# Performance work log

Hardware: AMD Instinct MI355X
Metric: run time of the kernel (lower is better)

The kernel has to match this reference:

```python
import jax, jax.numpy as jnp
import numpy as np

N = 100000; E = 1600000; D_IN = 128; HID = 64; HEADS = 2; OUT = 2; B = 8192
NEG_SLOPE = 0.2


def gat_conv(x, edge_index, W, a_src, a_dst, bias):
    """PyG-style GATConv with add_self_loops=True, concat=False (mean over heads).
    x: [N, Fin], W: [Fin, H*C], a_src/a_dst: [H, C], bias: [C]."""
    n = x.shape[0]
    H, C = a_src.shape
    h = (x @ W).reshape(n, H, C)                      # [N,H,C]
    s_src = (h * a_src[None]).sum(-1)                 # [N,H]
    s_dst = (h * a_dst[None]).sum(-1)                 # [N,H]
    loop = jnp.arange(n, dtype=edge_index.dtype)
    src = jnp.concatenate([edge_index[0], loop])      # [E+N]
    dst = jnp.concatenate([edge_index[1], loop])
    e = jax.nn.leaky_relu(s_src[src] + s_dst[dst], NEG_SLOPE)   # [E+N,H]
    # segment softmax over edges grouped by destination node
    m = jax.ops.segment_max(e, dst, num_segments=n)             # [N,H]
    ex = jnp.exp(e - m[dst])
    z = jax.ops.segment_sum(ex, dst, num_segments=n)            # [N,H]
    alpha = ex / z[dst]                                          # [E+N,H]
    msg = h[src] * alpha[:, :, None]                             # [E+N,H,C]
    out = jax.ops.segment_sum(msg, dst, num_segments=n)         # [N,H,C]
    return out.mean(axis=1) + bias                               # concat=False -> mean over heads


def setup_inputs() -> dict:
    key = jax.random.key(0)
    ks = jax.random.split(key, 32)
    def p(k, shape, fan_in):
        return (jax.random.normal(k, shape, dtype=jnp.float32) / np.sqrt(fan_in)).astype(jnp.float32)
    inp = {}
    inp["x_l"] = jax.random.normal(ks[0], (N, D_IN), dtype=jnp.float32)
    inp["x_r"] = jax.random.normal(ks[1], (N, D_IN), dtype=jnp.float32)
    inp["edge_index_l"] = jax.random.randint(ks[2], (2, E), 0, N, dtype=jnp.int64 if jax.config.jax_enable_x64 else jnp.int32)
    inp["edge_index_r"] = jax.random.randint(ks[3], (2, E), 0, N, dtype=jnp.int64 if jax.config.jax_enable_x64 else jnp.int32)
    inp["labels_l"] = jax.random.randint(ks[4], (B,), 0, N)
    inp["labels_r"] = jax.random.randint(ks[5], (B,), 0, N)
    i = 6
    for side in ("l", "r"):
        inp[f"w1{side}"] = p(ks[i], (D_IN, HEADS * HID), D_IN); i += 1
        inp[f"as1{side}"] = p(ks[i], (HEADS, HID), HID); i += 1
        inp[f"ad1{side}"] = p(ks[i], (HEADS, HID), HID); i += 1
        inp[f"b1{side}"] = jnp.zeros((HID,), jnp.float32)
        inp[f"w2{side}"] = p(ks[i], (HID, HEADS * HID), HID); i += 1
        inp[f"as2{side}"] = p(ks[i], (HEADS, HID), HID); i += 1
        inp[f"ad2{side}"] = p(ks[i], (HEADS, HID), HID); i += 1
        inp[f"b2{side}"] = jnp.zeros((HID,), jnp.float32)
    inp["fc1_w"] = p(ks[i], (2 * HID, HID), 2 * HID); i += 1
    inp["fc1_b"] = jnp.zeros((HID,), jnp.float32)
    inp["fc2_w"] = p(ks[i], (HID, OUT), HID); i += 1
    inp["fc2_b"] = jnp.zeros((OUT,), jnp.float32)
    return inp


def reference(x_l, x_r, edge_index_l, edge_index_r, labels_l, labels_r,
              w1l, as1l, ad1l, b1l, w2l, as2l, ad2l, b2l,
              w1r, as1r, ad1r, b1r, w2r, as2r, ad2r, b2r,
              fc1_w, fc1_b, fc2_w, fc2_b):
    # left tower (dropout is identity in eval mode)
    hl = jax.nn.relu(gat_conv(x_l, edge_index_l, w1l, as1l, ad1l, b1l))
    hl = jax.nn.relu(gat_conv(hl, edge_index_l, w2l, as2l, ad2l, b2l))
    # right tower
    hr = jax.nn.relu(gat_conv(x_r, edge_index_r, w1r, as1r, ad1r, b1r))
    hr = jax.nn.relu(gat_conv(hr, edge_index_r, w2r, as2r, ad2r, b2r))
    # merge_graphs: gather node features per labeled pair, concat
    merged = jnp.concatenate([hl[labels_l], hr[labels_r]], axis=-1)  # [B, 2*HID]
    x = jax.nn.relu(merged @ fc1_w + fc1_b)
    return x @ fc2_w + fc2_b
```

## Files before the change

### kernel.cpp

```cpp
#include <hip/hip_runtime.h>
#include <hip/hip_bf16.h>
#include <hip/hip_fp16.h>

constexpr int NN   = 100000;
constexpr int EE   = 1600000;
constexpr int BB   = 8192;
constexpr int PAD  = 48;
constexpr float NEG_SLOPE = 0.2f;

constexpr int GBM = 128;
constexpr int GB = (NN + GBM - 1) / GBM;
constexpr int AB2 = NN / 8;

constexpr int BSPAN = 256;
constexpr int NB    = (NN + BSPAN - 1) / BSPAN;
constexpr int BCAP  = 5120;
constexpr int CHA   = 2048;
constexpr int NCH   = (EE + CHA - 1) / CHA;

typedef _Float16 f16x8 __attribute__((ext_vector_type(8)));
typedef _Float16 f16x4 __attribute__((ext_vector_type(4)));
typedef float    f32x4 __attribute__((ext_vector_type(4)));

__device__ __forceinline__ float4 ld4(const float* p) { return *(const float4*)p; }

template <typename TIN, int K>
__device__ __forceinline__
void gemm_mfma_body(int bid, const TIN* __restrict__ x,
                    const __half* __restrict__ Wimg,
                    const float* __restrict__ a_src, const float* __restrict__ a_dst,
                    __half* __restrict__ h,
                    float* __restrict__ ssrc, float* __restrict__ sdst,
                    char* lds) {
    constexpr bool HAS_LO = sizeof(TIN) == 4;
    char* const xh = lds;
    char* const xl = HAS_LO ? (lds + 8192) : lds;
    char* const wh = lds + (HAS_LO ? 16384 : 8192);
    char* const wl = wh + 8192;

    const int tid = threadIdx.x;
    const int wid = tid >> 6;
    const int lane = tid & 63;
    const int l15 = lane & 15;
    const int lg = lane >> 4;
    const int row0 = bid * GBM;

    f32x4 acc[2][8];
    #pragma unroll
    for (int i = 0; i < 2; ++i)
        #pragma unroll
        for (int j = 0; j < 8; ++j) acc[i][j] = (f32x4)0.f;

    for (int kt = 0; kt < K; kt += 32) {
        __syncthreads();
        if constexpr (HAS_LO) {
            #pragma unroll
            for (int i = 0; i < 4; ++i) {
                int idx = tid + i * 256;
                int row = idx >> 3, c4 = idx & 7;
                int grow = row0 + row; if (grow >= NN) grow = NN - 1;
                float4 v = ld4(&x[(size_t)grow * K + kt + c4 * 4]);
                f16x4 hv, lv;
                float f0 = v.x; _Float16 h0 = (_Float16)f0; hv[0] = h0; lv[0] = (_Float16)(f0 - (float)h0);
                float f1 = v.y; _Float16 h1 = (_Float16)f1; hv[1] = h1; lv[1] = (_Float16)(f1 - (float)h1);
                float f2 = v.z; _Float16 h2 = (_Float16)f2; hv[2] = h2; lv[2] = (_Float16)(f2 - (float)h2);
                float f3 = v.w; _Float16 h3 = (_Float16)f3; hv[3] = h3; lv[3] = (_Float16)(f3 - (float)h3);
                int byt = row * 64 + ((c4 * 8) ^ ((row & 3) << 4));
                *(f16x4*)(xh + byt) = hv;
                *(f16x4*)(xl + byt) = lv;
            }
        } else {
            #pragma unroll
            for (int i = 0; i < 2; ++i) {
                int idx = tid + i * 256;
                int row = idx >> 2, c8 = idx & 3;
                int grow = row0 + row; if (grow >= NN) grow = NN - 1;
                uint4 v = *(const uint4*)&x[(size_t)grow * 64 + kt + c8 * 8];
                int byt = row * 64 + ((c8 * 16) ^ ((row & 3) << 4));
                *(uint4*)(xh + byt) = v;
            }
        }
        {
            const uint4* ws = (const uint4*)((const char*)Wimg + (size_t)(kt >> 5) * 16384);
            uint4* wd = (uint4*)wh;
            #pragma unroll
            for (int i = 0; i < 4; ++i) wd[tid + i * 256] = ws[tid + i * 256];
        }
        __syncthreads();

        const int koff = lg * 16;
        f16x8 ah[2], al[2];
        #pragma unroll
        for (int rt = 0; rt < 2; ++rt) {
            int row = wid * 32 + rt * 16 + l15;
            int byt = row * 64 + (koff ^ ((row & 3) << 4));
            ah[rt] = *(const f16x8*)(xh + byt);
            if constexpr (HAS_LO) al[rt] = *(const f16x8*)(xl + byt);
        }
        #pragma unroll
        for (int ct = 0; ct < 8; ++ct) {
            int col = ct * 16 + l15;
            int byt = col * 64 + (koff ^ ((col & 3) << 4));
            f16x8 bh = *(const f16x8*)(wh + byt);
            f16x8 bl = *(const f16x8*)(wl + byt);
            #pragma unroll
            for (int rt = 0; rt < 2; ++rt) {
                acc[rt][ct] = __builtin_amdgcn_mfma_f32_16x16x32_f16(ah[rt], bh, acc[rt][ct], 0, 0, 0);
                acc[rt][ct] = __builtin_amdgcn_mfma_f32_16x16x32_f16(ah[rt], bl, acc[rt][ct], 0, 0, 0);
                if constexpr (HAS_LO)
                    acc[rt][ct] = __builtin_amdgcn_mfma_f32_16x16x32_f16(al[rt], bh, acc[rt][ct], 0, 0, 0);
            }
        }
    }

    float sv[8], dv[8];
    #pragma unroll
    for (int ct = 0; ct < 8; ++ct) {
        sv[ct] = a_src[ct * 16 + l15];
        dv[ct] = a_dst[ct * 16 + l15];
    }
    #pragma unroll
    for (int rt = 0; rt < 2; ++rt) {
        #pragma unroll
        for (int r = 0; r < 4; ++r) {
            int row = row0 + wid * 32 + rt * 16 + lg * 4 + r;
            bool ok = row < NN;
            if (ok) {
                #pragma unroll
                for (int ct = 0; ct < 8; ++ct)
                    h[(size_t)row * 128 + ct * 16 + l15] = __float2half(acc[rt][ct][r]);
            }
            float ps0 = 0.f, pd0 = 0.f, ps1 = 0.f, pd1 = 0.f;
            #pragma unroll
            for (int ct = 0; ct < 4; ++ct) {
                ps0 = fmaf(acc[rt][ct][r], sv[ct], ps0);
                pd0 = fmaf(acc[rt][ct][r], dv[ct], pd0);
                ps1 = fmaf(acc[rt][ct + 4][r], sv[ct + 4], ps1);
                pd1 = fmaf(acc[rt][ct + 4][r], dv[ct + 4], pd1);
            }
            ps0 += __shfl_xor(ps0, 1); pd0 += __shfl_xor(pd0, 1);
            ps1 += __shfl_xor(ps1, 1); pd1 += __shfl_xor(pd1, 1);
            ps0 += __shfl_xor(ps0, 2); pd0 += __shfl_xor(pd0, 2);
            ps1 += __shfl_xor(ps1, 2); pd1 += __shfl_xor(pd1, 2);
            ps0 += __shfl_xor(ps0, 4); pd0 += __shfl_xor(pd0, 4);
            ps1 += __shfl_xor(ps1, 4); pd1 += __shfl_xor(pd1, 4);
            ps0 += __shfl_xor(ps0, 8); pd0 += __shfl_xor(pd0, 8);
            ps1 += __shfl_xor(ps1, 8); pd1 += __shfl_xor(pd1, 8);
            if (ok && l15 == 0) {
                ssrc[row * 2 + 0] = ps0;
                ssrc[row * 2 + 1] = ps1;
                sdst[row * 2 + 0] = pd0;
                sdst[row * 2 + 1] = pd1;
            }
        }
    }
}

__global__ __launch_bounds__(256)
void k_bucket(const int* __restrict__ el, const int* __restrict__ er,
              int* __restrict__ buf, int* __restrict__ gcur,
              const float* __restrict__ w1l, const float* __restrict__ w1r,
              const float* __restrict__ w2l, const float* __restrict__ w2r,
              __half* __restrict__ wi1l, __half* __restrict__ wi1r,
              __half* __restrict__ wi2l, __half* __restrict__ wi2r) {
    const int blk0 = blockIdx.x;
    if (blk0 >= 2 * NCH) {
        const int id = blk0 - 2 * NCH;
        const float* W;
        __half* img;
        int kt;
        if (id < 8) {
            W = (id >> 2) ? w1r : w1l;
            img = ((id >> 2) ? wi1r : wi1l) + (size_t)(id & 3) * 8192;
            kt = (id & 3) * 32;
        } else {
            int jx = id - 8;
            W = (jx >> 1) ? w2r : w2l;
            img = ((jx >> 1) ? wi2r : wi2l) + (size_t)(jx & 1) * 8192;
            kt = (jx & 1) * 32;
        }
        _Float16* imgh = (_Float16*)img;
        _Float16* imgl = imgh + 4096;
        for (int i = threadIdx.x; i < 4096; i += 256) {
            int kk = i >> 7, col = i & 127;
            float f = W[(size_t)(kt + kk) * 128 + col];
            _Float16 hi = (_Float16)f;
            _Float16 lo = (_Float16)(f - (float)hi);
            int hidx = col * 32 + (kk ^ ((col & 3) << 3));
            imgh[hidx] = hi;
            imgl[hidx] = lo;
        }
        return;
    }

    __shared__ int   P1[CHA];
    __shared__ short bkof[CHA];
    __shared__ int hist[NB];
    __shared__ int st[NB];
    __shared__ int ofs[NB];
    __shared__ int base[NB];
    __shared__ int sc[512];

    const int blk = blk0;
    const bool right = blk >= NCH;
    const int* __restrict__ e = right ? er : el;
    const int sideoff = right ? NB : 0;
    const int cbase = (right ? blk - NCH : blk) * CHA;
    int cnum = EE - cbase; if (cnum > CHA) cnum = CHA;
    const int t = threadIdx.x;

    for (int i = t; i < NB; i += 256) hist[i] = 0;
    __syncthreads();
    for (int i = t; i < cnum; i += 256) {
        int d = e[EE + cbase + i];
        atomicAdd(&hist[d >> 8], 1);
    }
    __syncthreads();

    sc[t]       = (t < NB)       ? hist[t]       : 0;
    sc[t + 256] = (t + 256 < NB) ? hist[t + 256] : 0;
    __syncthreads();
    for (int off = 1; off < 512; off <<= 1) {
        int a0 = sc[t];
        int a1 = sc[t + 256];
        int b0 = (t >= off)       ? sc[t - off]       : 0;
        int b1 = (t + 256 >= off) ? sc[t + 256 - off] : 0;
        __syncthreads();
        sc[t] = a0 + b0;
        sc[t + 256] = a1 + b1;
        __syncthreads();
    }
    for (int i = t; i < NB; i += 256) {
        int s = sc[i] - hist[i];
        st[i] = s;
        ofs[i] = s;
    }
    __syncthreads();
    for (int i = t; i < cnum; i += 256) {
        int d = e[EE + cbase + i];
        int s = e[cbase + i];
        int bk = d >> 8;
        int pos = atomicAdd(&ofs[bk], 1);
        P1[pos] = (s << 8) | (d & 255);
        bkof[pos] = (short)bk;
    }
    __syncthreads();
    for (int i = t; i < NB; i += 256)
        base[i] = hist[i] ? atomicAdd(&gcur[sideoff + i], hist[i]) : 0;
    __syncthreads();
    for (int j = t; j < cnum; j += 256) {
        int bk = bkof[j];
        buf[(size_t)(sideoff + bk) * BCAP + base[bk] + (j - st[bk])] = P1[j];
    }
}

__device__ __forceinline__
void csr_body(int blk, const int* __restrict__ buf, const int* __restrict__ gcur,
              int* __restrict__ cntl, int* __restrict__ cntr,
              int* __restrict__ csrl, int* __restrict__ csrr, char* smem) {
    int* lcnt = (int*)smem;
    int* lcsr = (int*)(smem + 1024);

    const bool right = blk >= NB;
    const int bk = right ? blk - NB : blk;
    int* __restrict__ cnt = right ? cntr : cntl;
    int* __restrict__ csr = right ? csrr : csrl;
    const int* __restrict__ src = buf + (size_t)blk * BCAP;
    const int count = gcur[blk];
    const int lo = bk * BSPAN;
    int nn = NN - lo; if (nn > BSPAN) nn = BSPAN;
    const int t = threadIdx.x;

    for (int i = t; i < nn; i += 256) lcnt[i] = 0;
    __syncthreads();
    for (int i = t; i < count; i += 256) {
        int v = src[i];
        int ld = v & 255;
        int s  = (int)((unsigned)v >> 8);
        int slot = atomicAdd(&lcnt[ld], 1);
        lcsr[ld * PAD + slot] = s;
    }
    __syncthreads();
    const int tot4 = (nn * PAD) >> 2;
    int4* __restrict__ dst4 = (int4*)&csr[(size_t)lo * PAD];
    const int4* __restrict__ s4 = (const int4*)lcsr;
    for (int i = t; i < tot4; i += 256) dst4[i] = s4[i];
    for (int i = t; i < nn; i += 256) cnt[lo + i] = lcnt[i];
}

__global__ __launch_bounds__(256)
void k_csr_gemm1(const int* __restrict__ buf, const int* __restrict__ gcur,
                 int* __restrict__ cnt_l, int* __restrict__ cnt_r,
                 int* __restrict__ csr_l, int* __restrict__ csr_r,
                 const float* __restrict__ x_l, const float* __restrict__ x_r,
                 const __half* __restrict__ wi1l, const float* __restrict__ as1l,
                 const float* __restrict__ ad1l,
                 const __half* __restrict__ wi1r, const float* __restrict__ as1r,
                 const float* __restrict__ ad1r,
                 __half* __restrict__ h_l, __half* __restrict__ h_r,
                 float* __restrict__ ssrc_l, float* __restrict__ sdst_l,
                 float* __restrict__ ssrc_r, float* __restrict__ sdst_r) {
    __shared__ __align__(16) char smem[50176];
    int b = blockIdx.x;
    if (b < 2 * NB) {
        csr_body(b, buf, gcur, cnt_l, cnt_r, csr_l, csr_r, smem);
    } else {
        b -= 2 * NB;
        if (b < GB)
            gemm_mfma_body<float, 128>(b, x_l, wi1l, as1l, ad1l,
                                       h_l, ssrc_l, sdst_l, smem);
        else
            gemm_mfma_body<float, 128>(b - GB, x_r, wi1r, as1r, ad1r,
                                       h_r, ssrc_r, sdst_r, smem);
    }
}

__global__ __launch_bounds__(256)
void k_gemm2x(const __half* __restrict__ f_l, const __half* __restrict__ f_r,
              const __half* __restrict__ wi2l, const float* __restrict__ as2l,
              const float* __restrict__ ad2l,
              const __half* __restrict__ wi2r, const float* __restrict__ as2r,
              const float* __restrict__ ad2r,
              __half* __restrict__ h_l, __half* __restrict__ h_r,
              float* __restrict__ ssrc_l, float* __restrict__ sdst_l,
              float* __restrict__ ssrc_r, float* __restrict__ sdst_r) {
    __shared__ __align__(16) char smem[24576];
    int b = blockIdx.x;
    if (b < GB)
        gemm_mfma_body<__half, 64>(b, (const __half*)f_l, wi2l, as2l, ad2l,
                                   h_l, ssrc_l, sdst_l, smem);
    else
        gemm_mfma_body<__half, 64>(b - GB, (const __half*)f_r, wi2r, as2r, ad2r,
                                   h_r, ssrc_r, sdst_r, smem);
}

__device__ __forceinline__
void att_body(int n, const __half* __restrict__ h,
              const float* __restrict__ ssrc, const float* __restrict__ sdst,
              const int* __restrict__ cnt, const int* __restrict__ csr,
              const float* __restrict__ bias, __half* __restrict__ out) {
    const int g  = threadIdx.x & 31;
    const int hs = g >> 4;
    const int j  = g & 15;
    const int ch = g * 4;

    float sd = sdst[n * 2 + hs];
    float es = ssrc[n * 2 + hs] + sd;
    es = es > 0.f ? es : NEG_SLOPE * es;
    const float wself = __expf(es);
    float zl = 0.f;

    uint2 sv = *(const uint2*)&h[(size_t)n * 128 + ch];
    __half2 sh0 = *(__half2*)&sv.x, sh1 = *(__half2*)&sv.y;
    float2 p01 = __half22float2(sh0), p23 = __half22float2(sh1);
    float a0 = wself * p01.x, a1 = wself * p01.y;
    float a2 = wself * p23.x, a3 = wself * p23.y;

    int b = n * PAD;
    const int e = b + cnt[n];
    while (b < e) {
        int c = e - b; if (c > 16) c = 16;
        int idx = b + (j < c ? j : c - 1);
        int sj = csr[idx];
        float ev = ssrc[sj * 2 + hs] + sd;
        ev = ev > 0.f ? ev : NEG_SLOPE * ev;
        float w = (j < c) ? __expf(ev) : 0.f;
        zl += w;
        int jj = 0;
        for (; jj + 4 <= c; jj += 4) {
            int s0 = __shfl(sj, jj,     32);
            int s1 = __shfl(sj, jj + 1, 32);
            int s2 = __shfl(sj, jj + 2, 32);
            int s3 = __shfl(sj, jj + 3, 32);
            float w0 = __shfl(w, hs * 16 + jj,     32);
            float w1 = __shfl(w, hs * 16 + jj + 1, 32);
            float w2 = __shfl(w, hs * 16 + jj + 2, 32);
            float w3 = __shfl(w, hs * 16 + jj + 3, 32);
            uint2 u0 = *(const uint2*)&h[(size_t)(unsigned)(s0 * 128 + ch)];
            uint2 u1 = *(const uint2*)&h[(size_t)(unsigned)(s1 * 128 + ch)];
            uint2 u2 = *(const uint2*)&h[(size_t)(unsigned)(s2 * 128 + ch)];
            uint2 u3 = *(const uint2*)&h[(size_t)(unsigned)(s3 * 128 + ch)];
            float2 f0a = __half22float2(*(__half2*)&u0.x), f0b = __half22float2(*(__half2*)&u0.y);
            float2 f1a = __half22float2(*(__half2*)&u1.x), f1b = __half22float2(*(__half2*)&u1.y);
            float2 f2a = __half22float2(*(__half2*)&u2.x), f2b = __half22float2(*(__half2*)&u2.y);
            float2 f3a = __half22float2(*(__half2*)&u3.x), f3b = __half22float2(*(__half2*)&u3.y);
            a0 = fmaf(w0, f0a.x, a0); a1 = fmaf(w0, f0a.y, a1);
            a2 = fmaf(w0, f0b.x, a2); a3 = fmaf(w0, f0b.y, a3);
            a0 = fmaf(w1, f1a.x, a0); a1 = fmaf(w1, f1a.y, a1);
            a2 = fmaf(w1, f1b.x, a2); a3 = fmaf(w1, f1b.y, a3);
            a0 = fmaf(w2, f2a.x, a0); a1 = fmaf(w2, f2a.y, a1);
            a2 = fmaf(w2, f2b.x, a2); a3 = fmaf(w2, f2b.y, a3);
            a0 = fmaf(w3, f3a.x, a0); a1 = fmaf(w3, f3a.y, a1);
            a2 = fmaf(w3, f3b.x, a2); a3 = fmaf(w3, f3b.y, a3);
        }
        for (; jj < c; ++jj) {
            int s0   = __shfl(sj, jj, 32);
            float w0 = __shfl(w, hs * 16 + jj, 32);
            uint2 u0 = *(const uint2*)&h[(size_t)(unsigned)(s0 * 128 + ch)];
            float2 f0a = __half22float2(*(__half2*)&u0.x), f0b = __half22float2(*(__half2*)&u0.y);
            a0 = fmaf(w0, f0a.x, a0); a1 = fmaf(w0, f0a.y, a1);
            a2 = fmaf(w0, f0b.x, a2); a3 = fmaf(w0, f0b.y, a3);
        }
        b += c;
    }

    zl += __shfl_xor(zl, 1, 32);
    zl += __shfl_xor(zl, 2, 32);
    zl += __shfl_xor(zl, 4, 32);
    zl += __shfl_xor(zl, 8, 32);
    const float z = wself + zl;

    float zi = 1.f / z;
    a0 *= zi; a1 *= zi; a2 *= zi; a3 *= zi;
    a0 = 0.5f * (a0 + __shfl_xor(a0, 16));
    a1 = 0.5f * (a1 + __shfl_xor(a1, 16));
    a2 = 0.5f * (a2 + __shfl_xor(a2, 16));
    a3 = 0.5f * (a3 + __shfl_xor(a3, 16));
    if (hs == 0) {
        float4 bv = *(const float4*)&bias[ch];
        a0 += bv.x; a1 += bv.y; a2 += bv.z; a3 += bv.w;
        a0 = a0 > 0.f ? a0 : 0.f;
        a1 = a1 > 0.f ? a1 : 0.f;
        a2 = a2 > 0.f ? a2 : 0.f;
        a3 = a3 > 0.f ? a3 : 0.f;
        __align__(8) __half2 hp[2];
        hp[0] = __floats2half2_rn(a0, a1);
        hp[1] = __floats2half2_rn(a2, a3);
        *(uint2*)&out[(size_t)n * 64 + ch] = *(uint2*)hp;
    }
}

__global__ __launch_bounds__(256)
void k_att2x(const __half* __restrict__ h_l, const __half* __restrict__ h_r,
             const float* __restrict__ ssrc_l, const float* __restrict__ sdst_l,
             const float* __restrict__ ssrc_r, const float* __restrict__ sdst_r,
             const int* __restrict__ cnt_l, const int* __restrict__ csr_l,
             const int* __restrict__ cnt_r, const int* __restrict__ csr_r,
             const float* __restrict__ bias_l, const float* __restrict__ bias_r,
             __half* __restrict__ feat_l, __half* __restrict__ feat_r) {
    int blk = blockIdx.x;
    bool right = blk >= AB2;
    int n = (blk - (right ? AB2 : 0)) * 8 + (threadIdx.x >> 5);
    if (!right) att_body(n, h_l, ssrc_l, sdst_l, cnt_l, csr_l, bias_l, feat_l);
    else        att_body(n, h_r, ssrc_r, sdst_r, cnt_r, csr_r, bias_r, feat_r);
}

__global__ __launch_bounds__(256)
void k_fc(const __half* __restrict__ fl, const __half* __restrict__ fr,
          const int* __restrict__ ll, const int* __restrict__ lr,
          const float* __restrict__ w1, const float* __restrict__ b1,
          const float* __restrict__ w2, const float* __restrict__ b2,
          float* __restrict__ out) {
    int b = blockIdx.x * 4 + (threadIdx.x >> 6);
    int j = threadIdx.x & 63;
    int la = ll[b], lb = lr[b];
    float v0 = __half2float(fl[(size_t)la * 64 + j]);
    float v1 = __half2float(fr[(size_t)lb * 64 + j]);
    float acc = b1[j];
    #pragma unroll 8
    for (int k = 0; k < 64; ++k)
        acc += __shfl(v0, k, 64) * w1[k * 64 + j];
    #pragma unroll 8
    for (int k = 0; k < 64; ++k)
        acc += __shfl(v1, k, 64) * w1[(64 + k) * 64 + j];
    float x1 = acc > 0.f ? acc : 0.f;
    float p0 = x1 * w2[j * 2 + 0];
    float p1 = x1 * w2[j * 2 + 1];
    #pragma unroll
    for (int o = 32; o >= 1; o >>= 1) {
        p0 += __shfl_xor(p0, o, 64);
        p1 += __shfl_xor(p1, o, 64);
    }
    if (j == 0) {
        out[b * 2 + 0] = p0 + b2[0];
        out[b * 2 + 1] = p1 + b2[1];
    }
}

extern "C" void kernel_launch(void* const* d_in, const int* in_sizes, int n_in,
                              void* d_out, int out_size, void* d_ws, size_t ws_size,
                              hipStream_t stream) {
    const float* x_l  = (const float*)d_in[0];
    const float* x_r  = (const float*)d_in[1];
    const int* ei_l  = (const int*)d_in[2];
    const int* ei_r  = (const int*)d_in[3];
    const int* lab_l = (const int*)d_in[4];
    const int* lab_r = (const int*)d_in[5];
    const float* w1l  = (const float*)d_in[6];
    const float* as1l = (const float*)d_in[7];
    const float* ad1l = (const float*)d_in[8];
    const float* b1l  = (const float*)d_in[9];
    const float* w2l  = (const float*)d_in[10];
    const float* as2l = (const float*)d_in[11];
    const float* ad2l = (const float*)d_in[12];
    const float* b2l  = (const float*)d_in[13];
    const float* w1r  = (const float*)d_in[14];
    const float* as1r = (const float*)d_in[15];
    const float* ad1r = (const float*)d_in[16];
    const float* b1r  = (const float*)d_in[17];
    const float* w2r  = (const float*)d_in[18];
    const float* as2r = (const float*)d_in[19];
    const float* ad2r = (const float*)d_in[20];
    const float* b2r  = (const float*)d_in[21];
    const float* fc1w = (const float*)d_in[22];
    const float* fc1b = (const float*)d_in[23];
    const float* fc2w = (const float*)d_in[24];
    const float* fc2b = (const float*)d_in[25];

    char* p = (char*)d_ws;
    auto alloc = [&](size_t bytes) -> void* {
        void* q = (void*)p;
        p += (bytes + 255) & ~(size_t)255;
        return q;
    };
    __half* h_l    = (__half*)alloc((size_t)NN * 128 * 2);
    __half* h_r    = (__half*)alloc((size_t)NN * 128 * 2);
    __half* feat_l = (__half*)alloc((size_t)NN * 64 * 2);
    __half* feat_r = (__half*)alloc((size_t)NN * 64 * 2);
    float* ssrc_l = (float*)alloc((size_t)NN * 2 * 4);
    float* sdst_l = (float*)alloc((size_t)NN * 2 * 4);
    float* ssrc_r = (float*)alloc((size_t)NN * 2 * 4);
    float* sdst_r = (float*)alloc((size_t)NN * 2 * 4);
    int* cnt2  = (int*)alloc(((size_t)2 * NN + 2 * NB) * 4);
    int* csr_l = (int*)alloc((size_t)NN * PAD * 4);
    int* csr_r = (int*)alloc((size_t)NN * PAD * 4);
    __half* wi1l = (__half*)alloc(65536);
    __half* wi1r = (__half*)alloc(65536);
    __half* wi2l = (__half*)alloc(32768);
    __half* wi2r = (__half*)alloc(32768);
    int* cnt_l = cnt2;
    int* cnt_r = cnt2 + NN;
    int* gcur  = cnt2 + 2 * NN;

    int* buf = (int*)feat_l;

    hipMemsetAsync(gcur, 0, (size_t)2 * NB * 4, stream);

    k_bucket<<<2 * NCH + 12, 256, 0, stream>>>(ei_l, ei_r, buf, gcur,
                                               w1l, w1r, w2l, w2r,
                                               wi1l, wi1r, wi2l, wi2r);

    k_csr_gemm1<<<2 * NB + 2 * GB, 256, 0, stream>>>(
        buf, gcur, cnt_l, cnt_r, csr_l, csr_r,
        x_l, x_r, wi1l, as1l, ad1l, wi1r, as1r, ad1r,
        h_l, h_r, ssrc_l, sdst_l, ssrc_r, sdst_r);

    k_att2x<<<2 * AB2, 256, 0, stream>>>(h_l, h_r, ssrc_l, sdst_l, ssrc_r, sdst_r,
                                         cnt_l, csr_l, cnt_r, csr_r,
                                         b1l, b1r, feat_l, feat_r);

    k_gemm2x<<<2 * GB, 256, 0, stream>>>(feat_l, feat_r,
                                         wi2l, as2l, ad2l, wi2r, as2r, ad2r,
                                         h_l, h_r, ssrc_l, sdst_l, ssrc_r, sdst_r);

    k_att2x<<<2 * AB2, 256, 0, stream>>>(h_l, h_r, ssrc_l, sdst_l, ssrc_r, sdst_r,
                                         cnt_l, csr_l, cnt_r, csr_r,
                                         b2l, b2r, feat_l, feat_r);

    k_fc<<<(BB + 3) / 4, 256, 0, stream>>>(feat_l, feat_r, lab_l, lab_r,
                                           fc1w, fc1b, fc2w, fc2b,
                                           (float*)d_out);
}
```

Measured before the change: 546.8 us.

## Fuse layer-1 attention aggregation with layer-2 GEMM via LDS staging

Adds a kernel that computes layer-1 GAT attention aggregation for a 64-row tile, writes the result as fp16 into swizzled shared memory, and immediately runs the layer-2 MFMA GEMM plus attention-score reduction on it. This removes the global round trip of the intermediate features and one kernel launch. The cost is a smaller GEMM tile, with the weight image reloaded for each 64-row block. The workspace needs extra buffers, so the old path is kept as a fallback when the workspace is too small.

```diff
diff --git a/kernel.cpp b/kernel.cpp
--- a/kernel.cpp
+++ b/kernel.cpp
@@ -10,6 +10,8 @@
 
 constexpr int GBM = 128;
 constexpr int GB = (NN + GBM - 1) / GBM;
+constexpr int GBM2 = 64;
+constexpr int GB2 = (NN + GBM2 - 1) / GBM2;
 constexpr int AB2 = NN / 8;
 
 constexpr int BSPAN = 256;
@@ -334,11 +336,13 @@
                                    h_r, ssrc_r, sdst_r, smem);
 }
 
+template <int WRITER>
 __device__ __forceinline__
-void att_body(int n, const __half* __restrict__ h,
-              const float* __restrict__ ssrc, const float* __restrict__ sdst,
-              const int* __restrict__ cnt, const int* __restrict__ csr,
-              const float* __restrict__ bias, __half* __restrict__ out) {
+void att_body_t(int n, int row_local, const __half* __restrict__ h,
+                const float* __restrict__ ssrc, const float* __restrict__ sdst,
+                const int* __restrict__ cnt, const int* __restrict__ csr,
+                const float* __restrict__ bias, __half* __restrict__ out,
+                char* featlds) {
     const int g  = threadIdx.x & 31;
     const int hs = g >> 4;
     const int j  = g & 15;
@@ -426,7 +430,14 @@
         __align__(8) __half2 hp[2];
         hp[0] = __floats2half2_rn(a0, a1);
         hp[1] = __floats2half2_rn(a2, a3);
-        *(uint2*)&out[(size_t)n * 64 + ch] = *(uint2*)hp;
+        if constexpr (WRITER == 0) {
+            *(uint2*)&out[(size_t)n * 64 + ch] = *(uint2*)hp;
+        } else {
+            int ph = ch >> 5;
+            int cc = ch & 31;
+            int byt = ph * (GBM2 * 64) + row_local * 64 + ((cc * 2) ^ ((row_local & 3) << 4));
+            *(uint2*)(featlds + byt) = *(uint2*)hp;
+        }
     }
 }
 
@@ -441,8 +452,137 @@
     int blk = blockIdx.x;
     bool right = blk >= AB2;
     int n = (blk - (right ? AB2 : 0)) * 8 + (threadIdx.x >> 5);
-    if (!right) att_body(n, h_l, ssrc_l, sdst_l, cnt_l, csr_l, bias_l, feat_l);
-    else        att_body(n, h_r, ssrc_r, sdst_r, cnt_r, csr_r, bias_r, feat_r);
+    if (!right) att_body_t<0>(n, 0, h_l, ssrc_l, sdst_l, cnt_l, csr_l, bias_l, feat_l, nullptr);
+    else        att_body_t<0>(n, 0, h_r, ssrc_r, sdst_r, cnt_r, csr_r, bias_r, feat_r, nullptr);
+}
+
+__global__ __launch_bounds__(256)
+void k_att1gemm2(const __half* __restrict__ h1_l, const __half* __restrict__ h1_r,
+                 const float* __restrict__ ss1_l, const float* __restrict__ sd1_l,
+                 const float* __restrict__ ss1_r, const float* __restrict__ sd1_r,
+                 const int* __restrict__ cnt_l, const int* __restrict__ csr_l,
+                 const int* __restrict__ cnt_r, const int* __restrict__ csr_r,
+                 const float* __restrict__ b1l, const float* __restrict__ b1r,
+                 const __half* __restrict__ wi2l, const float* __restrict__ as2l,
+                 const float* __restrict__ ad2l,
+                 const __half* __restrict__ wi2r, const float* __restrict__ as2r,
+                 const float* __restrict__ ad2r,
+                 __half* __restrict__ h2_l, __half* __restrict__ h2_r,
+                 float* __restrict__ ss2_l, float* __restrict__ sd2_l,
+                 float* __restrict__ ss2_r, float* __restrict__ sd2_r) {
+    __shared__ __align__(16) char smem[GBM2 * 64 * 2 + 16384];
+    char* const featp = smem;
+    char* const wh = smem + GBM2 * 64 * 2;
+    char* const wl = wh + 8192;
+
+    int b = blockIdx.x;
+    const bool right = b >= GB2;
+    const int bid = right ? b - GB2 : b;
+    const int row0 = bid * GBM2;
+
+    const __half* __restrict__ h1   = right ? h1_r : h1_l;
+    const float* __restrict__ ss1   = right ? ss1_r : ss1_l;
+    const float* __restrict__ sd1   = right ? sd1_r : sd1_l;
+    const int* __restrict__ cnt     = right ? cnt_r : cnt_l;
+    const int* __restrict__ csr     = right ? csr_r : csr_l;
+    const float* __restrict__ bias1 = right ? b1r : b1l;
+    const __half* __restrict__ Wimg = right ? wi2r : wi2l;
+    const float* __restrict__ a_src = right ? as2r : as2l;
+    const float* __restrict__ a_dst = right ? ad2r : ad2l;
+    __half* __restrict__ h2         = right ? h2_r : h2_l;
+    float* __restrict__ ss2         = right ? ss2_r : ss2_l;
+    float* __restrict__ sd2         = right ? sd2_r : sd2_l;
+
+    const int tid = threadIdx.x;
+
+    if (row0 + GBM2 > NN) {
+        for (int i = tid; i < (GBM2 * 64 * 2) / 16; i += 256)
+            ((uint4*)featp)[i] = make_uint4(0, 0, 0, 0);
+        __syncthreads();
+    }
+
+    #pragma unroll 1
+    for (int it = 0; it < GBM2 / 8; ++it) {
+        int nl = it * 8 + (tid >> 5);
+        int n = row0 + nl;
+        if (n < NN)
+            att_body_t<1>(n, nl, h1, ss1, sd1, cnt, csr, bias1, nullptr, featp);
+    }
+    __syncthreads();
+
+    const int wid = tid >> 6;
+    const int lane = tid & 63;
+    const int l15 = lane & 15;
+    const int lg = lane >> 4;
+
+    f32x4 acc[8];
+    #pragma unroll
+    for (int j = 0; j < 8; ++j) acc[j] = (f32x4)0.f;
+
+    #pragma unroll
+    for (int kp = 0; kp < 2; ++kp) {
+        if (kp) __syncthreads();
+        {
+            const uint4* ws = (const uint4*)((const char*)Wimg + (size_t)kp * 16384);
+            uint4* wd = (uint4*)wh;
+            #pragma unroll
+            for (int i = 0; i < 4; ++i) wd[tid + i * 256] = ws[tid + i * 256];
+        }
+        __syncthreads();
+
+        const int koff = lg * 16;
+        int row = wid * 16 + l15;
+        f16x8 ah = *(const f16x8*)(featp + kp * (GBM2 * 64) + row * 64 +
+                                   (koff ^ ((row & 3) << 4)));
+        #pragma unroll
+        for (int ct = 0; ct < 8; ++ct) {
+            int col = ct * 16 + l15;
+            int byt = col * 64 + (koff ^ ((col & 3) << 4));
+            f16x8 bh = *(const f16x8*)(wh + byt);
+            f16x8 bl = *(const f16x8*)(wl + byt);
+            acc[ct] = __builtin_amdgcn_mfma_f32_16x16x32_f16(ah, bh, acc[ct], 0, 0, 0);
+            acc[ct] = __builtin_amdgcn_mfma_f32_16x16x32_f16(ah, bl, acc[ct], 0, 0, 0);
+        }
+    }
+
+    float sv[8], dv[8];
+    #pragma unroll
+    for (int ct = 0; ct < 8; ++ct) {
+        sv[ct] = a_src[ct * 16 + l15];
+        dv[ct] = a_dst[ct * 16 + l15];
+    }
+    #pragma unroll
+    for (int r = 0; r < 4; ++r) {
+        int row = row0 + wid * 16 + lg * 4 + r;
+        bool ok = row < NN;
+        if (ok) {
+            #pragma unroll
+            for (int ct = 0; ct < 8; ++ct)
+                h2[(size_t)row * 128 + ct * 16 + l15] = __float2half(acc[ct][r]);
+        }
+        float ps0 = 0.f, pd0 = 0.f, ps1 = 0.f, pd1 = 0.f;
+        #pragma unroll
+        for (int ct = 0; ct < 4; ++ct) {
+            ps0 = fmaf(acc[ct][r], sv[ct], ps0);
+            pd0 = fmaf(acc[ct][r], dv[ct], pd0);
+            ps1 = fmaf(acc[ct + 4][r], sv[ct + 4], ps1);
+            pd1 = fmaf(acc[ct + 4][r], dv[ct + 4], pd1);
+        }
+        ps0 += __shfl_xor(ps0, 1); pd0 += __shfl_xor(pd0, 1);
+        ps1 += __shfl_xor(ps1, 1); pd1 += __shfl_xor(pd1, 1);
+        ps0 += __shfl_xor(ps0, 2); pd0 += __shfl_xor(pd0, 2);
+        ps1 += __shfl_xor(ps1, 2); pd1 += __shfl_xor(pd1, 2);
+        ps0 += __shfl_xor(ps0, 4); pd0 += __shfl_xor(pd0, 4);
+        ps1 += __shfl_xor(ps1, 4); pd1 += __shfl_xor(pd1, 4);
+        ps0 += __shfl_xor(ps0, 8); pd0 += __shfl_xor(pd0, 8);
+        ps1 += __shfl_xor(ps1, 8); pd1 += __shfl_xor(pd1, 8);
+        if (ok && l15 == 0) {
+            ss2[row * 2 + 0] = ps0;
+            ss2[row * 2 + 1] = ps1;
+            sd2[row * 2 + 0] = pd0;
+            sd2[row * 2 + 1] = pd1;
+        }
+    }
 }
 
 __global__ __launch_bounds__(256)
@@ -513,14 +653,19 @@
         p += (bytes + 255) & ~(size_t)255;
         return q;
     };
+
     __half* h_l    = (__half*)alloc((size_t)NN * 128 * 2);
     __half* h_r    = (__half*)alloc((size_t)NN * 128 * 2);
-    __half* feat_l = (__half*)alloc((size_t)NN * 64 * 2);
-    __half* feat_r = (__half*)alloc((size_t)NN * 64 * 2);
+    __half* h2_l   = (__half*)alloc((size_t)NN * 128 * 2);
+    __half* h2_r   = (__half*)alloc((size_t)NN * 128 * 2);
     float* ssrc_l = (float*)alloc((size_t)NN * 2 * 4);
     float* sdst_l = (float*)alloc((size_t)NN * 2 * 4);
     float* ssrc_r = (float*)alloc((size_t)NN * 2 * 4);
     float* sdst_r = (float*)alloc((size_t)NN * 2 * 4);
+    float* ss2_l  = (float*)alloc((size_t)NN * 2 * 4);
+    float* sd2_l  = (float*)alloc((size_t)NN * 2 * 4);
+    float* ss2_r  = (float*)alloc((size_t)NN * 2 * 4);
+    float* sd2_r  = (float*)alloc((size_t)NN * 2 * 4);
     int* cnt2  = (int*)alloc(((size_t)2 * NN + 2 * NB) * 4);
     int* csr_l = (int*)alloc((size_t)NN * PAD * 4);
     int* csr_r = (int*)alloc((size_t)NN * PAD * 4);
@@ -532,6 +677,59 @@
     int* cnt_r = cnt2 + NN;
     int* gcur  = cnt2 + 2 * NN;
 
+    const bool fused = (size_t)(p - (char*)d_ws) <= ws_size;
+
+    if (fused) {
+        int* buf = (int*)h2_l;
+        __half* featF_l = h_l;
+        __half* featF_r = h_r;
+
+        hipMemsetAsync(gcur, 0, (size_t)2 * NB * 4, stream);
+
+        k_bucket<<<2 * NCH + 12, 256, 0, stream>>>(ei_l, ei_r, buf, gcur,
+                                                   w1l, w1r, w2l, w2r,
+                                                   wi1l, wi1r, wi2l, wi2r);
+
+        k_csr_gemm1<<<2 * NB + 2 * GB, 256, 0, stream>>>(
+            buf, gcur, cnt_l, cnt_r, csr_l, csr_r,
+            x_l, x_r, wi1l, as1l, ad1l, wi1r, as1r, ad1r,
+            h_l, h_r, ssrc_l, sdst_l, ssrc_r, sdst_r);
+
+        k_att1gemm2<<<2 * GB2, 256, 0, stream>>>(
+            h_l, h_r, ssrc_l, sdst_l, ssrc_r, sdst_r,
+            cnt_l, csr_l, cnt_r, csr_r, b1l, b1r,
+            wi2l, as2l, ad2l, wi2r, as2r, ad2r,
+            h2_l, h2_r, ss2_l, sd2_l, ss2_r, sd2_r);
+
+        k_att2x<<<2 * AB2, 256, 0, stream>>>(h2_l, h2_r, ss2_l, sd2_l, ss2_r, sd2_r,
+                                             cnt_l, csr_l, cnt_r, csr_r,
+                                             b2l, b2r, featF_l, featF_r);
+
+        k_fc<<<(BB + 3) / 4, 256, 0, stream>>>(featF_l, featF_r, lab_l, lab_r,
+                                               fc1w, fc1b, fc2w, fc2b,
+                                               (float*)d_out);
+        return;
+    }
+
+    p = (char*)d_ws;
+    h_l    = (__half*)alloc((size_t)NN * 128 * 2);
+    h_r    = (__half*)alloc((size_t)NN * 128 * 2);
+    __half* feat_l = (__half*)alloc((size_t)NN * 64 * 2);
+    __half* feat_r = (__half*)alloc((size_t)NN * 64 * 2);
+    ssrc_l = (float*)alloc((size_t)NN * 2 * 4);
+    sdst_l = (float*)alloc((size_t)NN * 2 * 4);
+    ssrc_r = (float*)alloc((size_t)NN * 2 * 4);
+    sdst_r = (float*)alloc((size_t)NN * 2 * 4);
+    cnt2  = (int*)alloc(((size_t)2 * NN + 2 * NB) * 4);
+    csr_l = (int*)alloc((size_t)NN * PAD * 4);
+    csr_r = (int*)alloc((size_t)NN * PAD * 4);
+    wi1l = (__half*)alloc(65536);
+    wi1r = (__half*)alloc(65536);
+    wi2l = (__half*)alloc(32768);
+    wi2r = (__half*)alloc(32768);
+    cnt_l = cnt2;
+    cnt_r = cnt2 + NN;
+    gcur  = cnt2 + 2 * NN;
     int* buf = (int*)feat_l;
 
     hipMemsetAsync(gcur, 0, (size_t)2 * NB * 4, stream);
```

After: 598.3 us. 1.09x slower.

## Pre-split layer-1 inputs to fp16 hi/lo inside the bucketing kernel

Applied to the files above, without the earlier changes.

Adds 512 extra blocks to the edge-bucketing kernel that convert x_l and x_r from fp32 into separate fp16 hi and lo arrays in workspace. The layer-1 GEMM then loads these pre-split halves directly, so it no longer converts fp32 to fp16 inside its tile loop. The intent is to overlap the conversion with the bucketing work and lighten the GEMM's load path. In exchange it writes and rereads 4x25.6MB of extra fp16 data, and it falls back to the old path when the workspace is too small.

```diff
diff --git a/kernel.cpp b/kernel.cpp
--- a/kernel.cpp
+++ b/kernel.cpp
@@ -17,6 +17,7 @@
 constexpr int BCAP  = 5120;
 constexpr int CHA   = 2048;
 constexpr int NCH   = (EE + CHA - 1) / CHA;
+constexpr int XSB   = 512;
 
 typedef _Float16 f16x8 __attribute__((ext_vector_type(8)));
 typedef _Float16 f16x4 __attribute__((ext_vector_type(4)));
@@ -24,95 +25,12 @@
 
 __device__ __forceinline__ float4 ld4(const float* p) { return *(const float4*)p; }
 
-template <typename TIN, int K>
 __device__ __forceinline__
-void gemm_mfma_body(int bid, const TIN* __restrict__ x,
-                    const __half* __restrict__ Wimg,
-                    const float* __restrict__ a_src, const float* __restrict__ a_dst,
-                    __half* __restrict__ h,
-                    float* __restrict__ ssrc, float* __restrict__ sdst,
-                    char* lds) {
-    constexpr bool HAS_LO = sizeof(TIN) == 4;
-    char* const xh = lds;
-    char* const xl = HAS_LO ? (lds + 8192) : lds;
-    char* const wh = lds + (HAS_LO ? 16384 : 8192);
-    char* const wl = wh + 8192;
-
-    const int tid = threadIdx.x;
-    const int wid = tid >> 6;
-    const int lane = tid & 63;
-    const int l15 = lane & 15;
-    const int lg = lane >> 4;
-    const int row0 = bid * GBM;
-
-    f32x4 acc[2][8];
-    #pragma unroll
-    for (int i = 0; i < 2; ++i)
-        #pragma unroll
-        for (int j = 0; j < 8; ++j) acc[i][j] = (f32x4)0.f;
-
-    for (int kt = 0; kt < K; kt += 32) {
-        __syncthreads();
-        if constexpr (HAS_LO) {
-            #pragma unroll
-            for (int i = 0; i < 4; ++i) {
-                int idx = tid + i * 256;
-                int row = idx >> 3, c4 = idx & 7;
-                int grow = row0 + row; if (grow >= NN) grow = NN - 1;
-                float4 v = ld4(&x[(size_t)grow * K + kt + c4 * 4]);
-                f16x4 hv, lv;
-                float f0 = v.x; _Float16 h0 = (_Float16)f0; hv[0] = h0; lv[0] = (_Float16)(f0 - (float)h0);
-                float f1 = v.y; _Float16 h1 = (_Float16)f1; hv[1] = h1; lv[1] = (_Float16)(f1 - (float)h1);
-                float f2 = v.z; _Float16 h2 = (_Float16)f2; hv[2] = h2; lv[2] = (_Float16)(f2 - (float)h2);
-                float f3 = v.w; _Float16 h3 = (_Float16)f3; hv[3] = h3; lv[3] = (_Float16)(f3 - (float)h3);
-                int byt = row * 64 + ((c4 * 8) ^ ((row & 3) << 4));
-                *(f16x4*)(xh + byt) = hv;
-                *(f16x4*)(xl + byt) = lv;
-            }
-        } else {
-            #pragma unroll
-            for (int i = 0; i < 2; ++i) {
-                int idx = tid + i * 256;
-                int row = idx >> 2, c8 = idx & 3;
-                int grow = row0 + row; if (grow >= NN) grow = NN - 1;
-                uint4 v = *(const uint4*)&x[(size_t)grow * 64 + kt + c8 * 8];
-                int byt = row * 64 + ((c8 * 16) ^ ((row & 3) << 4));
-                *(uint4*)(xh + byt) = v;
-            }
-        }
-        {
-            const uint4* ws = (const uint4*)((const char*)Wimg + (size_t)(kt >> 5) * 16384);
-            uint4* wd = (uint4*)wh;
-            #pragma unroll
-            for (int i = 0; i < 4; ++i) wd[tid + i * 256] = ws[tid + i * 256];
-        }
-        __syncthreads();
-
-        const int koff = lg * 16;
-        f16x8 ah[2], al[2];
-        #pragma unroll
-        for (int rt = 0; rt < 2; ++rt) {
-            int row = wid * 32 + rt * 16 + l15;
-            int byt = row * 64 + (koff ^ ((row & 3) << 4));
-            ah[rt] = *(const f16x8*)(xh + byt);
-            if constexpr (HAS_LO) al[rt] = *(const f16x8*)(xl + byt);
-        }
-        #pragma unroll
-        for (int ct = 0; ct < 8; ++ct) {
-            int col = ct * 16 + l15;
-            int byt = col * 64 + (koff ^ ((col & 3) << 4));
-            f16x8 bh = *(const f16x8*)(wh + byt);
-            f16x8 bl = *(const f16x8*)(wl + byt);
-            #pragma unroll
-            for (int rt = 0; rt < 2; ++rt) {
-                acc[rt][ct] = __builtin_amdgcn_mfma_f32_16x16x32_f16(ah[rt], bh, acc[rt][ct], 0, 0, 0);
-                acc[rt][ct] = __builtin_amdgcn_mfma_f32_16x16x32_f16(ah[rt], bl, acc[rt][ct], 0, 0, 0);
-                if constexpr (HAS_LO)
-                    acc[rt][ct] = __builtin_amdgcn_mfma_f32_16x16x32_f16(al[rt], bh, acc[rt][ct], 0, 0, 0);
-            }
-        }
-    }
-
+void gemm_epilogue(int row0, int wid, int l15, int lg,
+                   f32x4 (&acc)[2][8],
+                   const float* __restrict__ a_src, const float* __restrict__ a_dst,
+                   __half* __restrict__ h,
+                   float* __restrict__ ssrc, float* __restrict__ sdst) {
     float sv[8], dv[8];
     #pragma unroll
     for (int ct = 0; ct < 8; ++ct) {
@@ -156,14 +74,200 @@
     }
 }
 
+template <typename TIN, int K>
+__device__ __forceinline__
+void gemm_mfma_body(int bid, const TIN* __restrict__ x,
+                    const __half* __restrict__ Wimg,
+                    const float* __restrict__ a_src, const float* __restrict__ a_dst,
+                    __half* __restrict__ h,
+                    float* __restrict__ ssrc, float* __restrict__ sdst,
+                    char* lds) {
+    constexpr bool HAS_LO = sizeof(TIN) == 4;
+    char* const xh = lds;
+    char* const xl = HAS_LO ? (lds + 8192) : lds;
+    char* const wh = lds + (HAS_LO ? 16384 : 8192);
+    char* const wl = wh + 8192;
+
+    const int tid = threadIdx.x;
+    const int wid = tid >> 6;
+    const int lane = tid & 63;
+    const int l15 = lane & 15;
+    const int lg = lane >> 4;
+    const int row0 = bid * GBM;
+
+    f32x4 acc[2][8];
+    #pragma unroll
+    for (int i = 0; i < 2; ++i)
+        #pragma unroll
+        for (int j = 0; j < 8; ++j) acc[i][j] = (f32x4)0.f;
+
+    for (int kt = 0; kt < K; kt += 32) {
+        __syncthreads();
+        if constexpr (HAS_LO) {
+            #pragma unroll
+            for (int i = 0; i < 4; ++i) {
+                int idx = tid + i * 256;
+                int row = idx >> 3, c4 = idx & 7;
+                int grow = row0 + row; if (grow >= NN) grow = NN - 1;
+                float4 v = ld4(&x[(size_t)grow * K + kt + c4 * 4]);
+                f16x4 hv, lv;
+                float f0 = v.x; _Float16 h0 = (_Float16)f0; hv[0] = h0; lv[0] = (_Float16)(f0 - (float)h0);
+                float f1 = v.y; _Float16 h1 = (_Float16)f1; hv[1] = h1; lv[1] = (_Float16)(f1 - (float)h1);
+                float f2 = v.z; _Float16 h2 = (_Float16)f2; hv[2] = h2; lv[2] = (_Float16)(f2 - (float)h2);
+                float f3 = v.w; _Float16 h3 = (_Float16)f3; hv[3] = h3; lv[3] = (_Float16)(f3 - (float)h3);
+                int byt = row * 64 + ((c4 * 8) ^ ((row & 3) << 4));
+                *(f16x4*)(xh + byt) = hv;
+                *(f16x4*)(xl + byt) = lv;
+            }
+        } else {
+            #pragma unroll
+            for (int i = 0; i < 2; ++i) {
+                int idx = tid + i * 256;
+                int row = idx >> 2, c8 = idx & 3;
+                int grow = row0 + row; if (grow >= NN) grow = NN - 1;
+                uint4 v = *(const uint4*)&x[(size_t)grow * 64 + kt + c8 * 8];
+                int byt = row * 64 + ((c8 * 16) ^ ((row & 3) << 4));
+                *(uint4*)(xh + byt) = v;
+            }
+        }
+        {
+            const uint4* ws = (const uint4*)((const char*)Wimg + (size_t)(kt >> 5) * 16384);
+            uint4* wd = (uint4*)wh;
+            #pragma unroll
+            for (int i = 0; i < 4; ++i) wd[tid + i * 256] = ws[tid + i * 256];
+        }
+        __syncthreads();
+
+        const int koff = lg * 16;
+        f16x8 ah[2], al[2];
+        #pragma unroll
+        for (int rt = 0; rt < 2; ++rt) {
+            int row = wid * 32 + rt * 16 + l15;
+            int byt = row * 64 + (koff ^ ((row & 3) << 4));
+            ah[rt] = *(const f16x8*)(xh + byt);
+            if constexpr (HAS_LO) al[rt] = *(const f16x8*)(xl + byt);
+        }
+        #pragma unroll
+        for (int ct = 0; ct < 8; ++ct) {
+            int col = ct * 16 + l15;
+            int byt = col * 64 + (koff ^ ((col & 3) << 4));
+            f16x8 bh = *(const f16x8*)(wh + byt);
+            f16x8 bl = *(const f16x8*)(wl + byt);
+            #pragma unroll
+            for (int rt = 0; rt < 2; ++rt) {
+                acc[rt][ct] = __builtin_amdgcn_mfma_f32_16x16x32_f16(ah[rt], bh, acc[rt][ct], 0, 0, 0);
+                acc[rt][ct] = __builtin_amdgcn_mfma_f32_16x16x32_f16(ah[rt], bl, acc[rt][ct], 0, 0, 0);
+                if constexpr (HAS_LO)
+                    acc[rt][ct] = __builtin_amdgcn_mfma_f32_16x16x32_f16(al[rt], bh, acc[rt][ct], 0, 0, 0);
+            }
+        }
+    }
+    gemm_epilogue(row0, wid, l15, lg, acc, a_src, a_dst, h, ssrc, sdst);
+}
+
+__device__ __forceinline__
+void gemm_ps_body(int bid, const _Float16* __restrict__ xh_g,
+                  const _Float16* __restrict__ xl_g,
+                  const __half* __restrict__ Wimg,
+                  const float* __restrict__ a_src, const float* __restrict__ a_dst,
+                  __half* __restrict__ h,
+                  float* __restrict__ ssrc, float* __restrict__ sdst,
+                  char* lds) {
+    char* const xh = lds;
+    char* const xl = lds + 8192;
+    char* const wh = lds + 16384;
+    char* const wl = wh + 8192;
+
+    const int tid = threadIdx.x;
+    const int wid = tid >> 6;
+    const int lane = tid & 63;
+    const int l15 = lane & 15;
+    const int lg = lane >> 4;
+    const int row0 = bid * GBM;
+
+    f32x4 acc[2][8];
+    #pragma unroll
+    for (int i = 0; i < 2; ++i)
+        #pragma unroll
+        for (int j = 0; j < 8; ++j) acc[i][j] = (f32x4)0.f;
+
+    for (int kt = 0; kt < 128; kt += 32) {
+        __syncthreads();
+        #pragma unroll
+        for (int i = 0; i < 2; ++i) {
+            int idx = tid + i * 256;
+            int row = idx >> 2, c8 = idx & 3;
+            int grow = row0 + row; if (grow >= NN) grow = NN - 1;
+            size_t src = (size_t)grow * 128 + kt + c8 * 8;
+            int byt = row * 64 + ((c8 * 16) ^ ((row & 3) << 4));
+            *(uint4*)(xh + byt) = *(const uint4*)&xh_g[src];
+            *(uint4*)(xl + byt) = *(const uint4*)&xl_g[src];
+        }
+        {
+            const uint4* ws = (const uint4*)((const char*)Wimg + (size_t)(kt >> 5) * 16384);
+            uint4* wd = (uint4*)wh;
+            #pragma unroll
+            for (int i = 0; i < 4; ++i) wd[tid + i * 256] = ws[tid + i * 256];
+        }
+        __syncthreads();
+
+        const int koff = lg * 16;
+        f16x8 ah[2], al[2];
+        #pragma unroll
+        for (int rt = 0; rt < 2; ++rt) {
+            int row = wid * 32 + rt * 16 + l15;
+            int byt = row * 64 + (koff ^ ((row & 3) << 4));
+            ah[rt] = *(const f16x8*)(xh + byt);
+            al[rt] = *(const f16x8*)(xl + byt);
+        }
+        #pragma unroll
+        for (int ct = 0; ct < 8; ++ct) {
+            int col = ct * 16 + l15;
+            int byt = col * 64 + (koff ^ ((col & 3) << 4));
+            f16x8 bh = *(const f16x8*)(wh + byt);
+            f16x8 bl = *(const f16x8*)(wl + byt);
+            #pragma unroll
+            for (int rt = 0; rt < 2; ++rt) {
+                acc[rt][ct] = __builtin_amdgcn_mfma_f32_16x16x32_f16(ah[rt], bh, acc[rt][ct], 0, 0, 0);
+                acc[rt][ct] = __builtin_amdgcn_mfma_f32_16x16x32_f16(ah[rt], bl, acc[rt][ct], 0, 0, 0);
+                acc[rt][ct] = __builtin_amdgcn_mfma_f32_16x16x32_f16(al[rt], bh, acc[rt][ct], 0, 0, 0);
+            }
+        }
+    }
+    gemm_epilogue(row0, wid, l15, lg, acc, a_src, a_dst, h, ssrc, sdst);
+}
+
 __global__ __launch_bounds__(256)
 void k_bucket(const int* __restrict__ el, const int* __restrict__ er,
               int* __restrict__ buf, int* __restrict__ gcur,
               const float* __restrict__ w1l, const float* __restrict__ w1r,
               const float* __restrict__ w2l, const float* __restrict__ w2r,
               __half* __restrict__ wi1l, __half* __restrict__ wi1r,
-              __half* __restrict__ wi2l, __half* __restrict__ wi2r) {
+              __half* __restrict__ wi2l, __half* __restrict__ wi2r,
+              const float* __restrict__ x_l, const float* __restrict__ x_r,
+              _Float16* __restrict__ xh_l, _Float16* __restrict__ xl_l,
+              _Float16* __restrict__ xh_r, _Float16* __restrict__ xl_r) {
     const int blk0 = blockIdx.x;
+    if (blk0 >= 2 * NCH + 12) {
+        const size_t TOT4 = (size_t)NN * 128 / 4;
+        for (size_t i = (size_t)(blk0 - (2 * NCH + 12)) * 256 + threadIdx.x;
+             i < 2 * TOT4; i += (size_t)XSB * 256) {
+            bool rt = i >= TOT4;
+            size_t j = rt ? i - TOT4 : i;
+            const float* xp = rt ? x_r : x_l;
+            _Float16* xhp = rt ? xh_r : xh_l;
+            _Float16* xlp = rt ? xl_r : xl_l;
+            float4 v = ld4(&xp[j * 4]);
+            f16x4 hv, lv;
+            float f0 = v.x; _Float16 h0 = (_Float16)f0; hv[0] = h0; lv[0] = (_Float16)(f0 - (float)h0);
+            float f1 = v.y; _Float16 h1 = (_Float16)f1; hv[1] = h1; lv[1] = (_Float16)(f1 - (float)h1);
+            float f2 = v.z; _Float16 h2 = (_Float16)f2; hv[2] = h2; lv[2] = (_Float16)(f2 - (float)h2);
+            float f3 = v.w; _Float16 h3 = (_Float16)f3; hv[3] = h3; lv[3] = (_Float16)(f3 - (float)h3);
+            *(f16x4*)&xhp[j * 4] = hv;
+            *(f16x4*)&xlp[j * 4] = lv;
+        }
+        return;
+    }
     if (blk0 >= 2 * NCH) {
         const int id = blk0 - 2 * NCH;
         const float* W;
@@ -286,6 +390,34 @@
     const int4* __restrict__ s4 = (const int4*)lcsr;
     for (int i = t; i < tot4; i += 256) dst4[i] = s4[i];
     for (int i = t; i < nn; i += 256) cnt[lo + i] = lcnt[i];
+}
+
+__global__ __launch_bounds__(256)
+void k_csr_gemm1_ps(const int* __restrict__ buf, const int* __restrict__ gcur,
+                    int* __restrict__ cnt_l, int* __restrict__ cnt_r,
+                    int* __restrict__ csr_l, int* __restrict__ csr_r,
+                    const _Float16* __restrict__ xh_l, const _Float16* __restrict__ xl_l,
+                    const _Float16* __restrict__ xh_r, const _Float16* __restrict__ xl_r,
+                    const __half* __restrict__ wi1l, const float* __restrict__ as1l,
+                    const float* __restrict__ ad1l,
+                    const __half* __restrict__ wi1r, const float* __restrict__ as1r,
+                    const float* __restrict__ ad1r,
+                    __half* __restrict__ h_l, __half* __restrict__ h_r,
+                    float* __restrict__ ssrc_l, float* __restrict__ sdst_l,
+                    float* __restrict__ ssrc_r, float* __restrict__ sdst_r) {
+    __shared__ __align__(16) char smem[50176];
+    int b = blockIdx.x;
+    if (b < 2 * NB) {
+        csr_body(b, buf, gcur, cnt_l, cnt_r, csr_l, csr_r, smem);
+    } else {
+        b -= 2 * NB;
+        if (b < GB)
+            gemm_ps_body(b, xh_l, xl_l, wi1l, as1l, ad1l,
+                         h_l, ssrc_l, sdst_l, smem);
+        else
+            gemm_ps_body(b - GB, xh_r, xl_r, wi1r, as1r, ad1r,
+                         h_r, ssrc_r, sdst_r, smem);
+    }
 }
 
 __global__ __launch_bounds__(256)
@@ -513,6 +645,7 @@
         p += (bytes + 255) & ~(size_t)255;
         return q;
     };
+
     __half* h_l    = (__half*)alloc((size_t)NN * 128 * 2);
     __half* h_r    = (__half*)alloc((size_t)NN * 128 * 2);
     __half* feat_l = (__half*)alloc((size_t)NN * 64 * 2);
@@ -531,19 +664,38 @@
     int* cnt_l = cnt2;
     int* cnt_r = cnt2 + NN;
     int* gcur  = cnt2 + 2 * NN;
-
     int* buf = (int*)feat_l;
 
+    _Float16* xh_l = (_Float16*)alloc((size_t)NN * 128 * 2);
+    _Float16* xl_l = (_Float16*)alloc((size_t)NN * 128 * 2);
+    _Float16* xh_r = (_Float16*)alloc((size_t)NN * 128 * 2);
+    _Float16* xl_r = (_Float16*)alloc((size_t)NN * 128 * 2);
+    const bool mainpath = (size_t)(p - (char*)d_ws) <= ws_size;
+
     hipMemsetAsync(gcur, 0, (size_t)2 * NB * 4, stream);
 
-    k_bucket<<<2 * NCH + 12, 256, 0, stream>>>(ei_l, ei_r, buf, gcur,
-                                               w1l, w1r, w2l, w2r,
-                                               wi1l, wi1r, wi2l, wi2r);
-
-    k_csr_gemm1<<<2 * NB + 2 * GB, 256, 0, stream>>>(
-        buf, gcur, cnt_l, cnt_r, csr_l, csr_r,
-        x_l, x_r, wi1l, as1l, ad1l, wi1r, as1r, ad1r,
-        h_l, h_r, ssrc_l, sdst_l, ssrc_r, sdst_r);
+    if (mainpath) {
+        k_bucket<<<2 * NCH + 12 + XSB, 256, 0, stream>>>(
+            ei_l, ei_r, buf, gcur, w1l, w1r, w2l, w2r,
+            wi1l, wi1r, wi2l, wi2r,
+            x_l, x_r, xh_l, xl_l, xh_r, xl_r);
+
+        k_csr_gemm1_ps<<<2 * NB + 2 * GB, 256, 0, stream>>>(
+            buf, gcur, cnt_l, cnt_r, csr_l, csr_r,
+            xh_l, xl_l, xh_r, xl_r,
+            wi1l, as1l, ad1l, wi1r, as1r, ad1r,
+            h_l, h_r, ssrc_l, sdst_l, ssrc_r, sdst_r);
+    } else {
+        k_bucket<<<2 * NCH + 12, 256, 0, stream>>>(
+            ei_l, ei_r, buf, gcur, w1l, w1r, w2l, w2r,
+            wi1l, wi1r, wi2l, wi2r,
+            x_l, x_r, nullptr, nullptr, nullptr, nullptr);
+
+        k_csr_gemm1<<<2 * NB + 2 * GB, 256, 0, stream>>>(
+            buf, gcur, cnt_l, cnt_r, csr_l, csr_r,
+            x_l, x_r, wi1l, as1l, ad1l, wi1r, as1r, ad1r,
+            h_l, h_r, ssrc_l, sdst_l, ssrc_r, sdst_r);
+    }
 
     k_att2x<<<2 * AB2, 256, 0, stream>>>(h_l, h_r, ssrc_l, sdst_l, ssrc_r, sdst_r,
                                          cnt_l, csr_l, cnt_r, csr_r,
```

Measured after the change: 589.3 us. 1.08x slower.
